# Performance work log

Measured on AMD Instinct MI355X. Metric: run time of the kernel, lower is better.

Reference implementation:

```python
import jax, jax.numpy as jnp
import numpy as np

N_NODES = 40000
N_EDGES = 640000
EMBED = 128
L = 3
EPS = 1e-5


def bn(x, g, b):
    # BatchNorm1d in training mode: batch mean / biased variance over axis 0
    m = jnp.mean(x, axis=0)
    v = jnp.var(x, axis=0)
    return (x - m) * jax.lax.rsqrt(v + EPS) * g + b


def setup_inputs() -> dict:
    key = jax.random.key(0)
    ks = jax.random.split(key, 16)
    d = {}
    d["node_attr"] = jax.random.normal(ks[0], (N_NODES, 2), jnp.float32)
    d["edge_index"] = jax.random.randint(ks[1], (2, N_EDGES), 0, N_NODES, jnp.int32)
    d["edge_attr"] = jax.random.normal(ks[2], (N_EDGES, 1), jnp.float32)
    s = 0.1
    d["W0"] = jax.random.normal(ks[3], (2, EMBED), jnp.float32) * s
    d["b0"] = jnp.zeros((EMBED,), jnp.float32)
    d["g0"] = jnp.ones((EMBED,), jnp.float32)
    d["bt0"] = jnp.zeros((EMBED,), jnp.float32)
    d["Wnode"] = jax.random.normal(ks[4], (L, EMBED, EMBED), jnp.float32) * s
    d["bnode"] = jnp.zeros((L, EMBED), jnp.float32)
    d["Wedge"] = jax.random.normal(ks[5], (L, 1, EMBED), jnp.float32) * s
    d["bedge"] = jnp.zeros((L, EMBED), jnp.float32)
    d["Wnb"] = jax.random.normal(ks[6], (L, EMBED, EMBED), jnp.float32) * s
    d["bnb"] = jnp.zeros((L, EMBED), jnp.float32)
    for nm in ("gn", "ge", "gnb", "gm1", "gm2"):
        d[nm] = jnp.ones((L, EMBED), jnp.float32)
    for nm in ("btn", "bte", "btnb", "btm1", "btm2"):
        d[nm] = jnp.zeros((L, EMBED), jnp.float32)
    d["Wm1"] = jax.random.normal(ks[7], (L, EMBED, EMBED), jnp.float32) * s
    d["bm1"] = jnp.zeros((L, EMBED), jnp.float32)
    d["Wm2"] = jax.random.normal(ks[8], (L, EMBED, EMBED), jnp.float32) * s
    d["bm2"] = jnp.zeros((L, EMBED), jnp.float32)
    return d


def reference(node_attr, edge_index, edge_attr,
              W0, b0, g0, bt0,
              Wnode, bnode, Wedge, bedge, Wnb, bnb,
              gn, btn, ge, bte, gnb, btnb,
              Wm1, bm1, gm1, btm1, Wm2, bm2, gm2, btm2):
    row, col = edge_index[0], edge_index[1]
    n = node_attr.shape[0]
    # initial node MLP (applied once, before layer 0)
    x = jax.nn.relu(bn(node_attr @ W0 + b0, g0, bt0))  # [N, E]
    for i in range(L):
        # edge branch: linear on raw edge_attr, scatter-add to source nodes (row)
        ea = edge_attr @ Wedge[i] + bedge[i]                      # [Ne, E]
        ea = jax.ops.segment_sum(ea, row, num_segments=n)         # [N, E]
        ea = bn(ea, ge[i], bte[i])
        # neighbor branch: h_j gathered from sources, aggregated at targets (col)
        h = x @ Wnb[i] + bnb[i]                                   # [N, E]
        aggr = jax.ops.segment_sum(h[row], col, num_segments=n)   # [N, E]
        # node branch
        xn = bn(x @ Wnode[i] + bnode[i], gn[i], btn[i])
        # update MLP
        y = jax.nn.relu(xn + bn(aggr, gnb[i], btnb[i]) + ea)
        y = jax.nn.relu(bn(y @ Wm1[i] + bm1[i], gm1[i], btm1[i]))
        y = jax.nn.relu(bn(y @ Wm2[i] + bm2[i], gm2[i], btm2[i]))
        x = y
    return x
```

## Files before the change

### kernel.cpp

```cpp
#include <hip/hip_runtime.h>

#define N_NODES 40000
#define N_EDGES 640000
#define EMB 128
#define NF ((size_t)N_NODES * EMB)
#define RCP_N (1.0f / (float)N_NODES)
#define BN_EPS 1e-5f
#define CAP 64
#define NSLICE 16
#define STB (NSLICE * 256)
#define GB 625

typedef _Float16 f16x8v __attribute__((ext_vector_type(8)));
typedef float f32x4v __attribute__((ext_vector_type(4)));
typedef unsigned short ushort8v __attribute__((ext_vector_type(8)));

__device__ __forceinline__ unsigned short f2h(float v) {
    return __builtin_bit_cast(unsigned short, (_Float16)v);
}
__device__ __forceinline__ float h2f(unsigned short u) {
    return (float)__builtin_bit_cast(_Float16, u);
}

__device__ __forceinline__ void bn_prep(
    const float* __restrict__ stat, const float* __restrict__ g,
    const float* __restrict__ bt, float* C, float* D, int t)
{
    if (t < 128) {
        float sm = 0.f, sq = 0.f;
        #pragma unroll
        for (int s = 0; s < NSLICE; ++s) {
            sm += stat[s * 256 + t];
            sq += stat[s * 256 + 128 + t];
        }
        float m = sm * RCP_N;
        float v = sq * RCP_N - m * m;
        float a = g[t] * rsqrtf(v + BN_EPS);
        C[t] = a; D[t] = bt[t] - m * a;
    }
}

__global__ __launch_bounds__(256) void edge_init_kernel(
    const float* __restrict__ na, const float* __restrict__ W0,
    const float* __restrict__ b0, unsigned short* __restrict__ Z,
    float* __restrict__ st,
    const int* __restrict__ ei, const float* __restrict__ ea,
    unsigned long long* __restrict__ scP, unsigned* __restrict__ cursor,
    unsigned short* __restrict__ slot,
    const float* __restrict__ Wnode, const float* __restrict__ Wnb,
    const float* __restrict__ Wm1, const float* __restrict__ Wm2,
    unsigned short* __restrict__ Wt)
{
    __shared__ float red[256];
    const int blk = blockIdx.x;
    const int t = threadIdx.x;
    if (blk < 625) {
        int col = t & 127, rh = t >> 7;
        float w0 = W0[col], w1 = W0[128 + col], bb = b0[col];
        int rbase = blk * 64;
        float sm = 0.f, sq = 0.f;
        #pragma unroll 4
        for (int i = 0; i < 32; ++i) {
            int r = rbase + rh + i * 2;
            float2 nv = *(const float2*)&na[r * 2];
            float v = fmaf(nv.x, w0, fmaf(nv.y, w1, bb));
            Z[(size_t)r * 128 + col] = f2h(v);
            sm += v; sq += v * v;
        }
        float* stS = st + (blk & (NSLICE - 1)) * 256;
        red[t] = sm; __syncthreads();
        if (t < 128) atomicAdd(&stS[t], red[t] + red[t + 128]);
        __syncthreads();
        red[t] = sq; __syncthreads();
        if (t < 128) atomicAdd(&stS[128 + t], red[t] + red[t + 128]);
    } else if (blk < 3125) {
        int e = (blk - 625) * 256 + t;
        int r = ei[e];
        int d = ei[N_EDGES + e];
        int fx = (int)rintf(ea[e] * 65536.0f);
        unsigned long long add =
            (((unsigned long long)(unsigned)(fx + 0x40000000)) << 20) | 1ULL;
        atomicAdd(&scP[r], add);
        unsigned pos = atomicAdd(&cursor[d], 1u);
        slot[(size_t)d * CAP + (pos < CAP ? pos : CAP - 1)] = (unsigned short)r;
    } else {
        int idx = blk - 3125;
        int mat = idx >> 3;
        int v = (idx & 7) * 256 + t;
        int kb = (v >> 7) * 8;
        int n = v & 127;
        int grp = mat / 3, lay = mat % 3;
        const float* src = (grp == 0) ? Wnode : (grp == 1) ? Wnb
                         : (grp == 2) ? Wm1 : Wm2;
        src += (size_t)lay * 16384;
        ushort8v o;
        #pragma unroll
        for (int j = 0; j < 8; ++j)
            o[j] = f2h(src[(size_t)(kb + j) * 128 + n]);
        *(ushort8v*)&Wt[(size_t)mat * 16384 + n * 128 + kb] = o;
    }
}

__global__ __launch_bounds__(256) void decode_kernel(
    const unsigned long long* __restrict__ scP, const unsigned* __restrict__ cursor,
    float* __restrict__ sN, float* __restrict__ cN, float* __restrict__ dgf,
    float* __restrict__ mom)
{
    int t = threadIdx.x;
    int i = blockIdx.x * 256 + t;
    float a0 = 0.f, a1 = 0.f, a2 = 0.f, a3 = 0.f, a4 = 0.f;
    if (i < N_NODES) {
        unsigned long long v = scP[i];
        unsigned cnt = (unsigned)(v & 0xFFFFFULL);
        long long sp = (long long)(v >> 20) - ((long long)cnt << 30);
        float s = (float)sp * (1.0f / 65536.0f);
        float c = (float)cnt;
        sN[i] = s; cN[i] = c;
        dgf[i] = (float)cursor[i];
        a0 = s; a1 = s * s; a2 = c; a3 = c * c; a4 = s * c;
    }
    #pragma unroll
    for (int off = 32; off > 0; off >>= 1) {
        a0 += __shfl_down(a0, off);
        a1 += __shfl_down(a1, off);
        a2 += __shfl_down(a2, off);
        a3 += __shfl_down(a3, off);
        a4 += __shfl_down(a4, off);
    }
    if ((t & 63) == 0) {
        atomicAdd(&mom[0], a0);
        atomicAdd(&mom[1], a1);
        atomicAdd(&mom[2], a2);
        atomicAdd(&mom[3], a3);
        atomicAdd(&mom[4], a4);
    }
}

__global__ __launch_bounds__(256) void gather_bn_kernel(
    const unsigned* __restrict__ cnt, const unsigned short* __restrict__ slot,
    const unsigned short* __restrict__ Ph,
    const float* __restrict__ stat, const float* __restrict__ g_in,
    const float* __restrict__ bt_in,
    unsigned short* __restrict__ Gh)
{
    __shared__ float aT[128], bT[128];
    int t = threadIdx.x;
    bn_prep(stat, g_in, bt_in, aT, bT, t);
    __syncthreads();
    int wid = (blockIdx.x * 256 + t) >> 6;
    int lane = t & 63;
    int q = lane >> 4, l16 = lane & 15;
    int cb = l16 * 8;
    float av[8], bv[8];
    #pragma unroll
    for (int k = 0; k < 8; ++k) { av[k] = aT[cb + k]; bv[k] = bT[cb + k]; }
    int n = (int)cnt[wid];
    n = n < CAP ? n : CAP;
    const unsigned short* sl = &slot[(size_t)wid * CAP];
    float s0[8] = {0}, s1[8] = {0};
    int j = q;
    for (; j + 4 < n; j += 8) {
        int r0 = sl[j], r1 = sl[j + 4];
        ushort8v v0 = *(const ushort8v*)&Ph[(size_t)r0 * 128 + cb];
        ushort8v v1 = *(const ushort8v*)&Ph[(size_t)r1 * 128 + cb];
        #pragma unroll
        for (int k = 0; k < 8; ++k) {
            s0[k] += fmaxf(0.f, fmaf(h2f(v0[k]), av[k], bv[k]));
            s1[k] += fmaxf(0.f, fmaf(h2f(v1[k]), av[k], bv[k]));
        }
    }
    for (; j < n; j += 4) {
        int r0 = sl[j];
        ushort8v v0 = *(const ushort8v*)&Ph[(size_t)r0 * 128 + cb];
        #pragma unroll
        for (int k = 0; k < 8; ++k)
            s0[k] += fmaxf(0.f, fmaf(h2f(v0[k]), av[k], bv[k]));
    }
    #pragma unroll
    for (int k = 0; k < 8; ++k) {
        float v = s0[k] + s1[k];
        v += __shfl_xor(v, 16);
        v += __shfl_xor(v, 32);
        s0[k] = v;
    }
    if (q == 0) {
        ushort8v o;
        #pragma unroll
        for (int k = 0; k < 8; ++k) o[k] = f2h(s0[k]);
        *(ushort8v*)&Gh[(size_t)wid * 128 + cb] = o;
    }
}

template<bool RSC>
__device__ __forceinline__ void gemm_core(
    int row0, int t, int slice, f16x8v afrag[4],
    const float* __restrict__ bias, const float* __restrict__ rowscale,
    unsigned short* __restrict__ Out, float* __restrict__ stats_out,
    const unsigned short* Bs, float (*redS)[128], float (*redQ)[128])
{
    const int w = t >> 6, lane = t & 63;
    const int la = lane & 15, lb = lane >> 4;
    const int kb = lb * 8;

    f32x4v acc[8];
    #pragma unroll
    for (int c = 0; c < 8; ++c) acc[c] = (f32x4v){0.f, 0.f, 0.f, 0.f};

    #pragma unroll
    for (int c = 0; c < 8; ++c) {
        int bn_ = (c << 4) + la;
        int bbase = bn_ * 128;
        int bswz = (bn_ & 7) << 3;
        #pragma unroll
        for (int s = 0; s < 4; ++s) {
            f16x8v bf = *(const f16x8v*)&Bs[(bbase + s * 32 + kb) ^ bswz];
            acc[c] = __builtin_amdgcn_mfma_f32_16x16x32_f16(
                afrag[s], bf, acc[c], 0, 0, 0);
        }
    }

    const int orow0 = row0 + (w << 4) + lb * 4;
    float rsj[4];
    if (RSC) {
        #pragma unroll
        for (int j = 0; j < 4; ++j) rsj[j] = rowscale[orow0 + j];
    }
    float csum[8], csq[8];
    #pragma unroll
    for (int c = 0; c < 8; ++c) {
        int col = (c << 4) + la;
        float bc = bias[col];
        float s0 = 0.f, s1 = 0.f;
        #pragma unroll
        for (int j = 0; j < 4; ++j) {
            float v = acc[c][j] + (RSC ? rsj[j] * bc : bc);
            Out[(size_t)(orow0 + j) * 128 + col] = f2h(v);
            s0 += v; s1 += v * v;
        }
        csum[c] = s0; csq[c] = s1;
    }
    #pragma unroll
    for (int c = 0; c < 8; ++c) {
        csum[c] += __shfl_xor(csum[c], 16);
        csum[c] += __shfl_xor(csum[c], 32);
        csq[c]  += __shfl_xor(csq[c], 16);
        csq[c]  += __shfl_xor(csq[c], 32);
    }
    if (lane < 16) {
        #pragma unroll
        for (int c = 0; c < 8; ++c) {
            redS[w][(c << 4) + lane] = csum[c];
            redQ[w][(c << 4) + lane] = csq[c];
        }
    }
    __syncthreads();
    float* stS = stats_out + slice * 256;
    if (t < 128) {
        atomicAdd(&stS[t], redS[0][t] + redS[1][t] + redS[2][t] + redS[3][t]);
        atomicAdd(&stS[128 + t], redQ[0][t] + redQ[1][t] + redQ[2][t] + redQ[3][t]);
    }
}

__device__ __forceinline__ void stage_B(
    const unsigned short* __restrict__ Wt, unsigned short* Bs, int t)
{
    #pragma unroll
    for (int i = 0; i < 8; ++i) {
        int cch = t + i * 256;
        int n = cch >> 4, off = (cch & 15) << 3;
        ushort8v w = *(const ushort8v*)&Wt[n * 128 + off];
        *(ushort8v*)&Bs[(n * 128 + off) ^ ((n & 7) << 3)] = w;
    }
}

template<int AMODE>
__device__ __forceinline__ void load_afrag_global(
    int row0, int t, f16x8v afrag[4],
    const unsigned short* __restrict__ A, const unsigned short* __restrict__ A2,
    const float* C1, const float* D1, const float* C2, const float* D2,
    const float* AE, const float* BE, const float* CE,
    const float* __restrict__ sN, const float* __restrict__ cN)
{
    const int w = t >> 6, lane = t & 63;
    const int la = lane & 15, lb = lane >> 4;
    const int ar = row0 + (w << 4) + la;
    const int kb = lb * 8;
    #pragma unroll
    for (int s = 0; s < 4; ++s) {
        ushort8v avv = *(const ushort8v*)&A[(size_t)ar * 128 + s * 32 + kb];
        if (AMODE == 0) {
            afrag[s] = __builtin_bit_cast(f16x8v, avv);
        } else if (AMODE == 1) {
            f16x8v o;
            #pragma unroll
            for (int j = 0; j < 8; ++j) {
                int qq = s * 32 + kb + j;
                o[j] = (_Float16)fmaxf(0.f, fmaf(h2f(avv[j]), C1[qq], D1[qq]));
            }
            afrag[s] = o;
        } else {
            ushort8v gv = *(const ushort8v*)&A2[(size_t)ar * 128 + s * 32 + kb];
            float sr = sN[ar], cr = cN[ar];
            f16x8v o;
            #pragma unroll
            for (int j = 0; j < 8; ++j) {
                int qq = s * 32 + kb + j;
                float y = h2f(avv[j]) * C1[qq] + D1[qq] + h2f(gv[j]) * C2[qq] + D2[qq]
                        + sr * AE[qq] + cr * BE[qq] + CE[qq];
                o[j] = (_Float16)fmaxf(0.f, y);
            }
            afrag[s] = o;
        }
    }
}

__global__ __launch_bounds__(256) void dual_gemm_kernel(
    const unsigned short* __restrict__ Ph, unsigned short* __restrict__ Gh,
    const unsigned short* __restrict__ WtZ, const unsigned short* __restrict__ WtG,
    const float* __restrict__ bZ, const float* __restrict__ bG,
    const float* __restrict__ dg,
    const float* __restrict__ st1, const float* __restrict__ g1,
    const float* __restrict__ bt1,
    unsigned short* __restrict__ ZNh,
    float* __restrict__ statZN, float* __restrict__ statG)
{
    __shared__ __align__(16) unsigned short Bs[128 * 128];
    __shared__ float C1[128], D1[128];
    __shared__ float redS[4][128], redQ[4][128];
    const int t = threadIdx.x;
    const int b = blockIdx.x;

    if (b < GB) {
        bn_prep(st1, g1, bt1, C1, D1, t);
        __syncthreads();
        const int row0 = b * 64;
        stage_B(WtZ, Bs, t);
        f16x8v afrag[4];
        load_afrag_global<1>(row0, t, afrag, Ph, nullptr,
                             C1, D1, nullptr, nullptr, nullptr, nullptr, nullptr,
                             nullptr, nullptr);
        __syncthreads();
        gemm_core<false>(row0, t, b & (NSLICE - 1), afrag, bZ, nullptr,
                         ZNh, statZN, Bs, redS, redQ);
    } else {
        const int row0 = (b - GB) * 64;
        stage_B(WtG, Bs, t);
        f16x8v afrag[4];
        load_afrag_global<0>(row0, t, afrag, Gh, nullptr,
                             nullptr, nullptr, nullptr, nullptr, nullptr,
                             nullptr, nullptr, nullptr, nullptr);
        __syncthreads();
        gemm_core<true>(row0, t, b & (NSLICE - 1), afrag, bG, dg,
                        Gh, statG, Bs, redS, redQ);
    }
}

template<int AMODE, bool RSC>
__global__ __launch_bounds__(256) void mfma_gemm_kernel(
    const unsigned short* __restrict__ A, const unsigned short* __restrict__ A2,
    const unsigned short* __restrict__ Wt,
    const float* __restrict__ bias, const float* __restrict__ rowscale,
    const float* __restrict__ st1, const float* __restrict__ g1, const float* __restrict__ bt1,
    const float* __restrict__ st2, const float* __restrict__ g2, const float* __restrict__ bt2,
    const float* __restrict__ sN, const float* __restrict__ cN,
    const float* __restrict__ scal,
    const float* __restrict__ We, const float* __restrict__ Be,
    const float* __restrict__ ge, const float* __restrict__ bte,
    unsigned short* __restrict__ Out, float* __restrict__ stats_out)
{
    __shared__ __align__(16) unsigned short Bs[128 * 128];
    __shared__ float C1[128], D1[128], C2[128], D2[128];
    __shared__ float AE[128], BE[128], CE[128];
    __shared__ float redS[4][128], redQ[4][128];
    const int t = threadIdx.x;

    if (AMODE >= 1) {
        bn_prep(st1, g1, bt1, C1, D1, t);
    }
    if (AMODE == 2) {
        bn_prep(st2, g2, bt2, C2, D2, t);
        if (t < 128) {
            float ms = scal[0] * RCP_N, vs = scal[1] * RCP_N - ms * ms;
            float mc = scal[2] * RCP_N, vc = scal[3] * RCP_N - mc * mc;
            float cov = scal[4] * RCP_N - ms * mc;
            float we = We[t], be = Be[t];
            float me = ms * we + mc * be;
            float ve = we * we * vs + be * be * vc + 2.f * we * be * cov;
            float ae = ge[t] * rsqrtf(ve + BN_EPS);
            AE[t] = we * ae; BE[t] = be * ae; CE[t] = bte[t] - me * ae;
        }
    }
    if (AMODE >= 1) __syncthreads();

    const int row0 = blockIdx.x * 64;
    stage_B(Wt, Bs, t);
    f16x8v afrag[4];
    load_afrag_global<AMODE>(row0, t, afrag, A, A2,
                             C1, D1, C2, D2, AE, BE, CE, sN, cN);
    __syncthreads();
    gemm_core<RSC>(row0, t, blockIdx.x & (NSLICE - 1), afrag, bias, rowscale,
                   Out, stats_out, Bs, redS, redQ);
}

__global__ __launch_bounds__(256) void bnrelu_kernel(
    const unsigned short* __restrict__ Z, const float* __restrict__ stz,
    const float* __restrict__ g, const float* __restrict__ bt,
    float* __restrict__ O)
{
    __shared__ float aT[128], bT[128];
    int t = threadIdx.x;
    bn_prep(stz, g, bt, aT, bT, t);
    __syncthreads();
    int stride = gridDim.x * 256;
    for (int idx = blockIdx.x * 256 + t; idx < N_NODES * 32; idx += stride) {
        int r = idx >> 5;
        int q = (idx & 31) * 4;
        ushort4 z = *(const ushort4*)&Z[(size_t)r * 128 + q];
        float4 o;
        o.x = fmaxf(0.f, fmaf(h2f(z.x), aT[q],     bT[q]));
        o.y = fmaxf(0.f, fmaf(h2f(z.y), aT[q + 1], bT[q + 1]));
        o.z = fmaxf(0.f, fmaf(h2f(z.z), aT[q + 2], bT[q + 2]));
        o.w = fmaxf(0.f, fmaf(h2f(z.w), aT[q + 3], bT[q + 3]));
        *(float4*)&O[(size_t)r * 128 + q] = o;
    }
}

extern "C" void kernel_launch(void* const* d_in, const int* in_sizes, int n_in,
                              void* d_out, int out_size, void* d_ws, size_t ws_size,
                              hipStream_t stream)
{
    const float* node_attr = (const float*)d_in[0];
    const int*   ei        = (const int*)d_in[1];
    const float* ea        = (const float*)d_in[2];
    const float* W0    = (const float*)d_in[3];
    const float* b0    = (const float*)d_in[4];
    const float* g0    = (const float*)d_in[5];
    const float* bt0   = (const float*)d_in[6];
    const float* Wnode = (const float*)d_in[7];
    const float* bnode = (const float*)d_in[8];
    const float* Wedge = (const float*)d_in[9];
    const float* bedge = (const float*)d_in[10];
    const float* Wnb   = (const float*)d_in[11];
    const float* bnb   = (const float*)d_in[12];
    const float* gn    = (const float*)d_in[13];
    const float* ge    = (const float*)d_in[14];
    const float* gnb   = (const float*)d_in[15];
    const float* gm1   = (const float*)d_in[16];
    const float* gm2   = (const float*)d_in[17];
    const float* btn   = (const float*)d_in[18];
    const float* bte   = (const float*)d_in[19];
    const float* btnb  = (const float*)d_in[20];
    const float* btm1  = (const float*)d_in[21];
    const float* btm2  = (const float*)d_in[22];
    const float* Wm1   = (const float*)d_in[23];
    const float* bm1   = (const float*)d_in[24];
    const float* Wm2   = (const float*)d_in[25];
    const float* bm2   = (const float*)d_in[26];
    float* out = (float*)d_out;

    unsigned short* Ph  = (unsigned short*)d_ws;
    unsigned short* ZNh = Ph + NF;
    unsigned short* Gh  = ZNh + NF;
    float* sN = (float*)(Gh + NF);
    float* cN = sN + N_NODES;
    float* dg = cN + N_NODES;
    float* st = dg + N_NODES;
    const size_t ST_FLOATS = 256 + (size_t)STB * 13;
    unsigned long long* scP = (unsigned long long*)(st + ST_FLOATS);
    unsigned* cursor = (unsigned*)(scP + N_NODES);
    unsigned short* slot = (unsigned short*)(cursor + N_NODES);
    unsigned short* Wtb = slot + (size_t)N_NODES * CAP;
    float* stInit = st + 256;
    float* layBase = st + 256 + STB;

    (void)hipMemsetAsync(st, 0, (ST_FLOATS + 3 * (size_t)N_NODES) * sizeof(float), stream);
    edge_init_kernel<<<3221, 256, 0, stream>>>(
        node_attr, W0, b0, Ph, stInit, ei, ea, scP, cursor, slot,
        Wnode, Wnb, Wm1, Wm2, Wtb);
    decode_kernel<<<157, 256, 0, stream>>>(scP, cursor, sN, cN, dg, st);

    const float* xst = stInit;
    const float* xg  = g0;
    const float* xbt = bt0;

    for (int i = 0; i < 3; ++i) {
        float* lay = layBase + (size_t)i * 4 * STB;
        gather_bn_kernel<<<10000, 256, 0, stream>>>(cursor, slot, Ph, xst, xg, xbt, Gh);
        dual_gemm_kernel<<<2 * GB, 256, 0, stream>>>(
            Ph, Gh,
            Wtb + (size_t)(0 + i) * 16384, Wtb + (size_t)(3 + i) * 16384,
            bnode + i * 128, bnb + i * 128, dg,
            xst, xg, xbt,
            ZNh, lay, lay + STB);
        mfma_gemm_kernel<2, false><<<GB, 256, 0, stream>>>(
            ZNh, Gh, Wtb + (size_t)(6 + i) * 16384, bm1 + i * 128, nullptr,
            lay, gn + i * 128, btn + i * 128,
            lay + STB, gnb + i * 128, btnb + i * 128,
            sN, cN, st,
            Wedge + i * 128, bedge + i * 128, ge + i * 128, bte + i * 128,
            ZNh, lay + 2 * STB);
        mfma_gemm_kernel<1, false><<<GB, 256, 0, stream>>>(
            ZNh, nullptr, Wtb + (size_t)(9 + i) * 16384, bm2 + i * 128, nullptr,
            lay + 2 * STB, gm1 + i * 128, btm1 + i * 128, nullptr, nullptr, nullptr,
            nullptr, nullptr, nullptr, nullptr, nullptr, nullptr, nullptr,
            Ph, lay + 3 * STB);

        xst = lay + 3 * STB;
        xg  = gm2 + i * 128;
        xbt = btm2 + i * 128;
    }
    bnrelu_kernel<<<2048, 256, 0, stream>>>(Ph, xst, xg, xbt, out);
}
```

Before: 309.2 us.

## Split GEMM tiles into 64-column halves and add separate output buffers

Each GEMM block now computes a 64x64 output tile instead of 64x128, which doubles the block count and halves the weight staged in LDS and the accumulator registers. Blocks that share a row tile now also read that A tile, so in-place outputs (Gh, ZNh) became unsafe. A new Qh buffer holds them and the later GEMMs write to alternating buffers. The aim is more parallelism and occupancy, at the cost of redundant A loads and repeated A-side BN/ReLU transforms.

```diff
diff --git a/kernel.cpp b/kernel.cpp
--- a/kernel.cpp
+++ b/kernel.cpp
@@ -9,7 +9,7 @@
 #define CAP 64
 #define NSLICE 16
 #define STB (NSLICE * 256)
-#define GB 625
+#define GBC 1250
 
 typedef _Float16 f16x8v __attribute__((ext_vector_type(8)));
 typedef float f32x4v __attribute__((ext_vector_type(4)));
@@ -193,24 +193,24 @@
 
 template<bool RSC>
 __device__ __forceinline__ void gemm_core(
-    int row0, int t, int slice, f16x8v afrag[4],
+    int row0, int col0, int t, int slice, f16x8v afrag[4],
     const float* __restrict__ bias, const float* __restrict__ rowscale,
     unsigned short* __restrict__ Out, float* __restrict__ stats_out,
-    const unsigned short* Bs, float (*redS)[128], float (*redQ)[128])
+    const unsigned short* Bs, float (*redS)[64], float (*redQ)[64])
 {
     const int w = t >> 6, lane = t & 63;
     const int la = lane & 15, lb = lane >> 4;
     const int kb = lb * 8;
 
-    f32x4v acc[8];
-    #pragma unroll
-    for (int c = 0; c < 8; ++c) acc[c] = (f32x4v){0.f, 0.f, 0.f, 0.f};
-
-    #pragma unroll
-    for (int c = 0; c < 8; ++c) {
-        int bn_ = (c << 4) + la;
-        int bbase = bn_ * 128;
-        int bswz = (bn_ & 7) << 3;
+    f32x4v acc[4];
+    #pragma unroll
+    for (int c = 0; c < 4; ++c) acc[c] = (f32x4v){0.f, 0.f, 0.f, 0.f};
+
+    #pragma unroll
+    for (int c = 0; c < 4; ++c) {
+        int nl = (c << 4) + la;
+        int bbase = nl * 128;
+        int bswz = (nl & 7) << 3;
         #pragma unroll
         for (int s = 0; s < 4; ++s) {
             f16x8v bf = *(const f16x8v*)&Bs[(bbase + s * 32 + kb) ^ bswz];
@@ -225,10 +225,10 @@
         #pragma unroll
         for (int j = 0; j < 4; ++j) rsj[j] = rowscale[orow0 + j];
     }
-    float csum[8], csq[8];
-    #pragma unroll
-    for (int c = 0; c < 8; ++c) {
-        int col = (c << 4) + la;
+    float csum[4], csq[4];
+    #pragma unroll
+    for (int c = 0; c < 4; ++c) {
+        int col = col0 + (c << 4) + la;
         float bc = bias[col];
         float s0 = 0.f, s1 = 0.f;
         #pragma unroll
@@ -240,7 +240,7 @@
         csum[c] = s0; csq[c] = s1;
     }
     #pragma unroll
-    for (int c = 0; c < 8; ++c) {
+    for (int c = 0; c < 4; ++c) {
         csum[c] += __shfl_xor(csum[c], 16);
         csum[c] += __shfl_xor(csum[c], 32);
         csq[c]  += __shfl_xor(csq[c], 16);
@@ -248,28 +248,28 @@
     }
     if (lane < 16) {
         #pragma unroll
-        for (int c = 0; c < 8; ++c) {
+        for (int c = 0; c < 4; ++c) {
             redS[w][(c << 4) + lane] = csum[c];
             redQ[w][(c << 4) + lane] = csq[c];
         }
     }
     __syncthreads();
     float* stS = stats_out + slice * 256;
-    if (t < 128) {
-        atomicAdd(&stS[t], redS[0][t] + redS[1][t] + redS[2][t] + redS[3][t]);
-        atomicAdd(&stS[128 + t], redQ[0][t] + redQ[1][t] + redQ[2][t] + redQ[3][t]);
+    if (t < 64) {
+        atomicAdd(&stS[col0 + t], redS[0][t] + redS[1][t] + redS[2][t] + redS[3][t]);
+        atomicAdd(&stS[128 + col0 + t], redQ[0][t] + redQ[1][t] + redQ[2][t] + redQ[3][t]);
     }
 }
 
 __device__ __forceinline__ void stage_B(
-    const unsigned short* __restrict__ Wt, unsigned short* Bs, int t)
-{
-    #pragma unroll
-    for (int i = 0; i < 8; ++i) {
-        int cch = t + i * 256;
-        int n = cch >> 4, off = (cch & 15) << 3;
-        ushort8v w = *(const ushort8v*)&Wt[n * 128 + off];
-        *(ushort8v*)&Bs[(n * 128 + off) ^ ((n & 7) << 3)] = w;
+    const unsigned short* __restrict__ Wt, int col0, unsigned short* Bs, int t)
+{
+    #pragma unroll
+    for (int i = 0; i < 4; ++i) {
+        int v = t + i * 256;
+        int nl = v >> 4, off = (v & 15) << 3;
+        ushort8v w = *(const ushort8v*)&Wt[(size_t)(col0 + nl) * 128 + off];
+        *(ushort8v*)&Bs[(nl * 128 + off) ^ ((nl & 7) << 3)] = w;
     }
 }
 
@@ -315,43 +315,44 @@
 }
 
 __global__ __launch_bounds__(256) void dual_gemm_kernel(
-    const unsigned short* __restrict__ Ph, unsigned short* __restrict__ Gh,
+    const unsigned short* __restrict__ Ph, const unsigned short* __restrict__ Gh,
     const unsigned short* __restrict__ WtZ, const unsigned short* __restrict__ WtG,
     const float* __restrict__ bZ, const float* __restrict__ bG,
     const float* __restrict__ dg,
     const float* __restrict__ st1, const float* __restrict__ g1,
     const float* __restrict__ bt1,
-    unsigned short* __restrict__ ZNh,
+    unsigned short* __restrict__ ZNh, unsigned short* __restrict__ Qh,
     float* __restrict__ statZN, float* __restrict__ statG)
 {
-    __shared__ __align__(16) unsigned short Bs[128 * 128];
+    __shared__ __align__(16) unsigned short Bs[64 * 128];
     __shared__ float C1[128], D1[128];
-    __shared__ float redS[4][128], redQ[4][128];
+    __shared__ float redS[4][64], redQ[4][64];
     const int t = threadIdx.x;
     const int b = blockIdx.x;
 
-    if (b < GB) {
+    if (b < GBC) {
         bn_prep(st1, g1, bt1, C1, D1, t);
         __syncthreads();
-        const int row0 = b * 64;
-        stage_B(WtZ, Bs, t);
+        const int row0 = (b >> 1) * 64, col0 = (b & 1) * 64;
+        stage_B(WtZ, col0, Bs, t);
         f16x8v afrag[4];
         load_afrag_global<1>(row0, t, afrag, Ph, nullptr,
                              C1, D1, nullptr, nullptr, nullptr, nullptr, nullptr,
                              nullptr, nullptr);
         __syncthreads();
-        gemm_core<false>(row0, t, b & (NSLICE - 1), afrag, bZ, nullptr,
+        gemm_core<false>(row0, col0, t, b & (NSLICE - 1), afrag, bZ, nullptr,
                          ZNh, statZN, Bs, redS, redQ);
     } else {
-        const int row0 = (b - GB) * 64;
-        stage_B(WtG, Bs, t);
+        const int bb = b - GBC;
+        const int row0 = (bb >> 1) * 64, col0 = (bb & 1) * 64;
+        stage_B(WtG, col0, Bs, t);
         f16x8v afrag[4];
         load_afrag_global<0>(row0, t, afrag, Gh, nullptr,
                              nullptr, nullptr, nullptr, nullptr, nullptr,
                              nullptr, nullptr, nullptr, nullptr);
         __syncthreads();
-        gemm_core<true>(row0, t, b & (NSLICE - 1), afrag, bG, dg,
-                        Gh, statG, Bs, redS, redQ);
+        gemm_core<true>(row0, col0, t, bb & (NSLICE - 1), afrag, bG, dg,
+                        Qh, statG, Bs, redS, redQ);
     }
 }
 
@@ -368,10 +369,10 @@
     const float* __restrict__ ge, const float* __restrict__ bte,
     unsigned short* __restrict__ Out, float* __restrict__ stats_out)
 {
-    __shared__ __align__(16) unsigned short Bs[128 * 128];
+    __shared__ __align__(16) unsigned short Bs[64 * 128];
     __shared__ float C1[128], D1[128], C2[128], D2[128];
     __shared__ float AE[128], BE[128], CE[128];
-    __shared__ float redS[4][128], redQ[4][128];
+    __shared__ float redS[4][64], redQ[4][64];
     const int t = threadIdx.x;
 
     if (AMODE >= 1) {
@@ -392,13 +393,13 @@
     }
     if (AMODE >= 1) __syncthreads();
 
-    const int row0 = blockIdx.x * 64;
-    stage_B(Wt, Bs, t);
+    const int row0 = (blockIdx.x >> 1) * 64, col0 = (blockIdx.x & 1) * 64;
+    stage_B(Wt, col0, Bs, t);
     f16x8v afrag[4];
     load_afrag_global<AMODE>(row0, t, afrag, A, A2,
                              C1, D1, C2, D2, AE, BE, CE, sN, cN);
     __syncthreads();
-    gemm_core<RSC>(row0, t, blockIdx.x & (NSLICE - 1), afrag, bias, rowscale,
+    gemm_core<RSC>(row0, col0, t, blockIdx.x & (NSLICE - 1), afrag, bias, rowscale,
                    Out, stats_out, Bs, redS, redQ);
 }
 
@@ -461,7 +462,8 @@
     unsigned short* Ph  = (unsigned short*)d_ws;
     unsigned short* ZNh = Ph + NF;
     unsigned short* Gh  = ZNh + NF;
-    float* sN = (float*)(Gh + NF);
+    unsigned short* Qh  = Gh + NF;
+    float* sN = (float*)(Qh + NF);
     float* cN = sN + N_NODES;
     float* dg = cN + N_NODES;
     float* st = dg + N_NODES;
@@ -486,21 +488,21 @@
     for (int i = 0; i < 3; ++i) {
         float* lay = layBase + (size_t)i * 4 * STB;
         gather_bn_kernel<<<10000, 256, 0, stream>>>(cursor, slot, Ph, xst, xg, xbt, Gh);
-        dual_gemm_kernel<<<2 * GB, 256, 0, stream>>>(
+        dual_gemm_kernel<<<2 * GBC, 256, 0, stream>>>(
             Ph, Gh,
             Wtb + (size_t)(0 + i) * 16384, Wtb + (size_t)(3 + i) * 16384,
             bnode + i * 128, bnb + i * 128, dg,
             xst, xg, xbt,
-            ZNh, lay, lay + STB);
-        mfma_gemm_kernel<2, false><<<GB, 256, 0, stream>>>(
-            ZNh, Gh, Wtb + (size_t)(6 + i) * 16384, bm1 + i * 128, nullptr,
+            ZNh, Qh, lay, lay + STB);
+        mfma_gemm_kernel<2, false><<<GBC, 256, 0, stream>>>(
+            ZNh, Qh, Wtb + (size_t)(6 + i) * 16384, bm1 + i * 128, nullptr,
             lay, gn + i * 128, btn + i * 128,
             lay + STB, gnb + i * 128, btnb + i * 128,
             sN, cN, st,
             Wedge + i * 128, bedge + i * 128, ge + i * 128, bte + i * 128,
-            ZNh, lay + 2 * STB);
-        mfma_gemm_kernel<1, false><<<GB, 256, 0, stream>>>(
-            ZNh, nullptr, Wtb + (size_t)(9 + i) * 16384, bm2 + i * 128, nullptr,
+            Gh, lay + 2 * STB);
+        mfma_gemm_kernel<1, false><<<GBC, 256, 0, stream>>>(
+            Gh, nullptr, Wtb + (size_t)(9 + i) * 16384, bm2 + i * 128, nullptr,
             lay + 2 * STB, gm1 + i * 128, btm1 + i * 128, nullptr, nullptr, nullptr,
             nullptr, nullptr, nullptr, nullptr, nullptr, nullptr, nullptr,
             Ph, lay + 3 * STB);
```

After: 323.4 us. 4.6% more time.
